# Kernel tuning notes

Measured on AMD Instinct MI355X. Metric: run time of the kernel, lower is better.

Reference implementation:

```python
import jax, jax.numpy as jnp
import numpy as np

NEG_NUM = -10000.0

def setup_inputs() -> dict:
    key = jax.random.key(0)
    k1, k2, k3, k4, k5, k6 = jax.random.split(key, 6)
    batch, enc_len = 32, 2048
    ctx_size, query_size, att_hid = 1024, 1024, 512
    in_dim = ctx_size + query_size
    ctx = jax.random.normal(k1, (batch, enc_len, ctx_size), dtype=jnp.float32)
    query = jax.random.normal(k2, (batch, query_size), dtype=jnp.float32)
    mask = jax.random.randint(k3, (batch, enc_len), 0, 2, dtype=jnp.int32)
    # Linear params (stored as (in, out) for x @ W + b)
    s1 = 1.0 / np.sqrt(in_dim)
    W1 = jax.random.uniform(k4, (in_dim, att_hid), jnp.float32, -s1, s1)
    b1 = jnp.zeros((att_hid,), jnp.float32)
    s2 = 1.0 / np.sqrt(att_hid)
    W2 = jax.random.uniform(k5, (att_hid, 1), jnp.float32, -s2, s2)
    b2 = jnp.zeros((1,), jnp.float32)
    return {"ctx": ctx, "query": query, "W1": W1, "b1": b1, "W2": W2, "b2": b2, "mask": mask}

def reference(ctx, query, W1, b1, W2, b2, mask):
    # ctx: (B, S, Dc), query: (B, Dq)
    B, S, Dc = ctx.shape
    Dq = query.shape[-1]
    # Equivalent to concat([ctx, query_expanded]) @ W1: split W1 into ctx/query blocks
    Wc, Wq = W1[:Dc], W1[Dc:]
    hidden = jnp.tanh(jnp.einsum('bsd,dh->bsh', ctx, Wc)
                      + (query @ Wq)[:, None, :] + b1)      # (B, S, H)
    score = jnp.einsum('bsh,h->bs', hidden, W2[:, 0]) + b2[0]  # (B, S)
    score = jnp.where(mask == 0, NEG_NUM, score)
    p_ctx = jax.nn.softmax(score, axis=-1)                   # (B, S)
    expected_ctx = jnp.einsum('bs,bsd->bd', p_ctx, ctx)      # (B, Dc)
    return (expected_ctx, p_ctx)
```

## Files before the change

kernel.cpp:

```cpp
#include <hip/hip_runtime.h>

typedef __bf16 bf16;
typedef __attribute__((ext_vector_type(8))) __bf16 bf16x8;
typedef __attribute__((ext_vector_type(4))) __bf16 bf16x4;
typedef __attribute__((ext_vector_type(4))) float f32x4;

#define B_  32
#define S_  2048
#define DC  1024
#define DQ  1024
#define H_  512
#define M_  (B_*S_)

#define BM  128
#define BN  512
#define BK  32
#define NCH 32

#define GLD16(g, l) __builtin_amdgcn_global_load_lds( \
    (__attribute__((address_space(1))) void*)(g),     \
    (__attribute__((address_space(3))) void*)(l), 16, 0, 0)

__global__ __launch_bounds__(256) void k_prep(const float* __restrict__ W1,
                                              const float* __restrict__ query,
                                              const float* __restrict__ b1,
                                              bf16* __restrict__ WcT2,
                                              float* __restrict__ qb) {
    const int bid = blockIdx.x, tid = threadIdx.x;
    if (bid < 256) {
        __shared__ bf16 t[32 * 68];
        const int kb = bid >> 3;
        const int cb = bid & 7;
        #pragma unroll
        for (int i = 0; i < 2; ++i) {
            int idx = i * 256 + tid;
            int k  = idx >> 4;
            int h4 = (idx & 15) * 4;
            const float4 v = *(const float4*)(W1 + ((size_t)(kb * 32 + k)) * H_ + cb * 64 + h4);
            bf16x4 pk = { (bf16)v.x, (bf16)v.y, (bf16)v.z, (bf16)v.w };
            *(bf16x4*)(&t[k * 68 + h4]) = pk;
        }
        __syncthreads();
        const int col = tid >> 2;
        const int kk0 = (tid & 3) * 8;
        bf16x8 o;
        #pragma unroll
        for (int j = 0; j < 8; ++j) o[j] = t[(kk0 + j) * 68 + col];
        const int kk0s = kk0 ^ (((col >> 1) & 3) << 3);
        *(bf16x8*)(WcT2 + (size_t)kb * 16384 + (size_t)(cb * 64 + col) * 32 + kk0s) = o;
    } else {
        const int r = bid - 256;
        const int hblk = r & 7;
        const int b    = r >> 3;
        __shared__ float q[DQ];
        __shared__ float red[256];
        #pragma unroll
        for (int i = 0; i < 4; ++i)
            q[tid + i * 256] = query[(size_t)b * DQ + tid + i * 256];
        __syncthreads();
        const int h  = hblk * 64 + (tid & 63);
        const int kc = tid >> 6;
        const float* w = W1 + (size_t)DC * H_ + (size_t)(kc * 256) * H_ + h;
        const float* qv = q + kc * 256;
        float acc = 0.0f;
        #pragma unroll 8
        for (int k = 0; k < 256; ++k)
            acc = fmaf(qv[k], w[(size_t)k * H_], acc);
        red[tid] = acc;
        __syncthreads();
        if (tid < 64)
            qb[(size_t)b * H_ + hblk * 64 + tid] =
                red[tid] + red[tid + 64] + red[tid + 128] + red[tid + 192] + b1[hblk * 64 + tid];
    }
}

__global__ __launch_bounds__(512, 2) void k_gemm(const float* __restrict__ ctx,
                                                 const bf16*  __restrict__ WcT2,
                                                 const float* __restrict__ qb,
                                                 const float* __restrict__ W2,
                                                 float* __restrict__ score) {
    __shared__ char smem_raw[147456];
    float* Af = (float*)smem_raw;
    bf16*  Bh = (bf16*)(smem_raw + 49152);
    float* red = (float*)smem_raw;

    const int tid  = threadIdx.x;
    const int mblk = blockIdx.x;
    const size_t row_base = (size_t)mblk * BM;
    const int b = mblk >> 4;

    const int lane = tid & 63;
    const int wv   = tid >> 6;
    const int wm   = wv & 1;
    const int wn   = wv >> 1;
    const int l16  = lane & 15;
    const int quad = lane >> 4;

    f32x4 acc[4][8] = {};

    const int arow0  = wv * 8 + (lane >> 3);
    const int acolsw = ((lane & 7) ^ ((lane >> 3) & 7)) * 4;
    const float* asrc0 = ctx + (row_base + arow0) * (size_t)DC + acolsw;
    const float* asrc1 = asrc0 + (size_t)64 * DC;
    const int adst0 = wv * 256 + lane * 4;
    const int adst1 = adst0 + 2048;
    const bf16* bsrcB = WcT2 + tid * 8;
    const int  boff   = tid * 8;

    const int a0 = (wm * 64 + l16) * 32 + (((quad * 2) ^ (l16 & 7)) * 4);
    const int b0 = (wn * 128 + l16) * 32 + ((quad * 8) ^ (((l16 >> 1) & 3) << 3));

#define KSTEP(KB, RD, WR, ISSUE)                                               \
  {                                                                            \
    if (ISSUE) {                                                               \
      _Pragma("unroll")                                                        \
      for (int i = 0; i < 4; ++i)                                              \
        GLD16(bsrcB + (size_t)((KB) + 2) * 16384 + i * 4096,                   \
              Bh + (WR) * 16384 + boff + i * 4096);                            \
      GLD16(asrc0 + (size_t)((KB) + 2) * 32, Af + (WR) * 4096 + adst0);        \
      GLD16(asrc1 + (size_t)((KB) + 2) * 32, Af + (WR) * 4096 + adst1);        \
    }                                                                          \
    bf16x8 aF[4], bF[8];                                                       \
    _Pragma("unroll")                                                          \
    for (int mf = 0; mf < 4; ++mf) {                                           \
      const f32x4 lo = *(const f32x4*)(Af + (RD) * 4096 + (a0 + mf * 512));    \
      const f32x4 hi = *(const f32x4*)(Af + (RD) * 4096 + ((a0 ^ 4) + mf * 512)); \
      bf16x8 t;                                                                \
      t[0] = (bf16)lo[0]; t[1] = (bf16)lo[1]; t[2] = (bf16)lo[2]; t[3] = (bf16)lo[3]; \
      t[4] = (bf16)hi[0]; t[5] = (bf16)hi[1]; t[6] = (bf16)hi[2]; t[7] = (bf16)hi[3]; \
      aF[mf] = t;                                                              \
    }                                                                          \
    _Pragma("unroll")                                                          \
    for (int nf = 0; nf < 8; ++nf)                                             \
      bF[nf] = *(const bf16x8*)(Bh + (RD) * 16384 + (b0 + nf * 512));          \
    __builtin_amdgcn_s_setprio(1);                                             \
    _Pragma("unroll")                                                          \
    for (int mf = 0; mf < 4; ++mf)                                             \
      _Pragma("unroll")                                                        \
      for (int nf = 0; nf < 8; ++nf)                                           \
        acc[mf][nf] = __builtin_amdgcn_mfma_f32_16x16x32_bf16(aF[mf], bF[nf],  \
                                                              acc[mf][nf], 0, 0, 0); \
    __builtin_amdgcn_s_setprio(0);                                             \
  }

#define WAITBAR(N)                                                             \
    asm volatile("s_waitcnt vmcnt(" #N ")" ::: "memory");                      \
    __builtin_amdgcn_s_barrier();                                              \
    __builtin_amdgcn_sched_barrier(0);

    #pragma unroll
    for (int i = 0; i < 4; ++i)
        GLD16(bsrcB + i * 4096, Bh + boff + i * 4096);
    GLD16(asrc0, Af + adst0);
    GLD16(asrc1, Af + adst1);
    #pragma unroll
    for (int i = 0; i < 4; ++i)
        GLD16(bsrcB + 16384 + i * 4096, Bh + 16384 + boff + i * 4096);
    GLD16(asrc0 + 32, Af + 4096 + adst0);
    GLD16(asrc1 + 32, Af + 4096 + adst1);
    WAITBAR(6)

    #pragma unroll 1
    for (int t3 = 0; t3 < 10; ++t3) {
        const int kb = t3 * 3;
        KSTEP(kb + 0, 0, 2, 1)
        WAITBAR(6)
        KSTEP(kb + 1, 1, 0, 1)
        WAITBAR(6)
        KSTEP(kb + 2, 2, 1, 1)
        WAITBAR(6)
    }
    KSTEP(30, 0, 0, 0)
    asm volatile("s_waitcnt vmcnt(0)" ::: "memory");
    __builtin_amdgcn_s_barrier();
    __builtin_amdgcn_sched_barrier(0);
    KSTEP(31, 1, 0, 0)
    __syncthreads();

#undef KSTEP
#undef WAITBAR

    float qv[8], wvv[8];
    #pragma unroll
    for (int nf = 0; nf < 8; ++nf) {
        int c = wn * 128 + nf * 16 + l16;
        qv[nf]  = qb[(size_t)b * H_ + c];
        wvv[nf] = W2[c];
    }
    #pragma unroll
    for (int mf = 0; mf < 4; ++mf) {
        #pragma unroll
        for (int r = 0; r < 4; ++r) {
            float s = 0.0f;
            #pragma unroll
            for (int nf = 0; nf < 8; ++nf) {
                float x = acc[mf][nf][r] + qv[nf];
                float t = 1.0f - 2.0f / (1.0f + __expf(2.0f * x));
                s = fmaf(t, wvv[nf], s);
            }
            s += __shfl_xor(s, 1);
            s += __shfl_xor(s, 2);
            s += __shfl_xor(s, 4);
            s += __shfl_xor(s, 8);
            if (l16 == 0)
                red[(wm * 64 + mf * 16 + quad * 4 + r) * 4 + wn] = s;
        }
    }
    __syncthreads();
    if (tid < BM)
        score[row_base + tid] = red[tid * 4] + red[tid * 4 + 1] + red[tid * 4 + 2] + red[tid * 4 + 3];
}

__global__ __launch_bounds__(256) void k_softmax(const float* __restrict__ score,
                                                 const float* __restrict__ b2,
                                                 const int*   __restrict__ mask,
                                                 float* __restrict__ p_out) {
    int b = blockIdx.x, tid = threadIdx.x;
    __shared__ float red[256];
    float loc[8];
    float b2v = b2[0];
    float mx = -1e30f;
    #pragma unroll
    for (int i = 0; i < 8; ++i) {
        size_t r = (size_t)b * S_ + i * 256 + tid;
        float v = score[r] + b2v;
        if (mask[r] == 0) v = -10000.0f;
        loc[i] = v;
        mx = fmaxf(mx, v);
    }
    red[tid] = mx; __syncthreads();
    for (int o = 128; o > 0; o >>= 1) {
        if (tid < o) red[tid] = fmaxf(red[tid], red[tid + o]);
        __syncthreads();
    }
    mx = red[0]; __syncthreads();
    float se = 0.0f;
    #pragma unroll
    for (int i = 0; i < 8; ++i) {
        float e = __expf(loc[i] - mx);
        loc[i] = e;
        se += e;
    }
    red[tid] = se; __syncthreads();
    for (int o = 128; o > 0; o >>= 1) {
        if (tid < o) red[tid] += red[tid + o];
        __syncthreads();
    }
    float inv = 1.0f / red[0];
    #pragma unroll
    for (int i = 0; i < 8; ++i)
        p_out[(size_t)b * S_ + i * 256 + tid] = loc[i] * inv;
}

__global__ __launch_bounds__(256) void k_expected(const float* __restrict__ ctx,
                                                  const float* __restrict__ p,
                                                  float* __restrict__ partial) {
    int b = blockIdx.x, ch = blockIdx.y, tid = threadIdx.x;
    __shared__ float ps[64];
    if (tid < 64) ps[tid] = p[(size_t)b * S_ + ch * 64 + tid];
    __syncthreads();
    const float* base = ctx + ((size_t)b * S_ + ch * 64) * DC + tid * 4;
    float ax = 0.f, ay = 0.f, az = 0.f, aw = 0.f;
    #pragma unroll 8
    for (int s = 0; s < 64; ++s) {
        const float4 v = *(const float4*)(base + (size_t)s * DC);
        float w = ps[s];
        ax = fmaf(w, v.x, ax);
        ay = fmaf(w, v.y, ay);
        az = fmaf(w, v.z, az);
        aw = fmaf(w, v.w, aw);
    }
    float4 o = { ax, ay, az, aw };
    *(float4*)(partial + ((size_t)(b * NCH + ch)) * DC + tid * 4) = o;
}

__global__ __launch_bounds__(256) void k_reduce(const float* __restrict__ partial,
                                                float* __restrict__ out) {
    int b = blockIdx.x, tid = threadIdx.x;
    float4 acc = { 0.f, 0.f, 0.f, 0.f };
    #pragma unroll
    for (int c = 0; c < NCH; ++c) {
        const float4 v = *(const float4*)(partial + ((size_t)(b * NCH + c)) * DC + tid * 4);
        acc.x += v.x; acc.y += v.y; acc.z += v.z; acc.w += v.w;
    }
    *(float4*)(out + (size_t)b * DC + tid * 4) = acc;
}

extern "C" void kernel_launch(void* const* d_in, const int* in_sizes, int n_in,
                              void* d_out, int out_size, void* d_ws, size_t ws_size,
                              hipStream_t stream) {
    (void)in_sizes; (void)n_in; (void)out_size; (void)ws_size;
    const float* ctx   = (const float*)d_in[0];
    const float* query = (const float*)d_in[1];
    const float* W1    = (const float*)d_in[2];
    const float* b1    = (const float*)d_in[3];
    const float* W2    = (const float*)d_in[4];
    const float* b2    = (const float*)d_in[5];
    const int*   mask  = (const int*)d_in[6];

    float* out      = (float*)d_out;
    float* expected = out;
    float* p_out    = out + 32768;

    char* w = (char*)d_ws;
    bf16*  WcT2      = (bf16*)w;
    float* qb        = (float*)(w + (1 << 20));
    float* score     = (float*)(w + (1 << 20) + (64 << 10));
    float* partial_e = (float*)(w + (1 << 20) + (320 << 10));

    k_prep    <<<512, 256, 0, stream>>>(W1, query, b1, WcT2, qb);
    k_gemm    <<<512, 512, 0, stream>>>(ctx, WcT2, qb, W2, score);
    k_softmax <<<B_, 256, 0, stream>>>(score, b2, mask, p_out);
    k_expected<<<dim3(B_, NCH), 256, 0, stream>>>(ctx, p_out, partial_e);
    k_reduce  <<<B_, 256, 0, stream>>>(partial_e, expected);
}
```

Before: 480.1 us.

## Compact unmasked rows and skip masked positions in GEMM and weighted sum

A new prep stage builds a per-batch list of unmasked sequence indices and counts via a prefix scan. The GEMM and expected-context kernels then process only those rows, gathering ctx rows through the index list, because masked scores are overwritten and their softmax weights underflow to zero. The aim is to roughly halve both the ctx traffic and the MFMA work. In exchange, A tiles are loaded straight into registers instead of through LDS, and the B swizzle is dropped, which may cause LDS bank conflicts. If a batch were fully masked, the results would differ from the uniform-softmax reference.

```diff
diff --git a/kernel.cpp b/kernel.cpp
--- a/kernel.cpp
+++ b/kernel.cpp
@@ -10,12 +10,8 @@
 #define DC  1024
 #define DQ  1024
 #define H_  512
-#define M_  (B_*S_)
-
-#define BM  128
-#define BN  512
-#define BK  32
-#define NCH 32
+#define NCH 16
+#define NBLK 16
 
 #define GLD16(g, l) __builtin_amdgcn_global_load_lds( \
     (__attribute__((address_space(1))) void*)(g),     \
@@ -24,8 +20,11 @@
 __global__ __launch_bounds__(256) void k_prep(const float* __restrict__ W1,
                                               const float* __restrict__ query,
                                               const float* __restrict__ b1,
+                                              const int*   __restrict__ mask,
                                               bf16* __restrict__ WcT2,
-                                              float* __restrict__ qb) {
+                                              float* __restrict__ qb,
+                                              int* __restrict__ glist,
+                                              int* __restrict__ cnts) {
     const int bid = blockIdx.x, tid = threadIdx.x;
     if (bid < 256) {
         __shared__ bf16 t[32 * 68];
@@ -46,9 +45,8 @@
         bf16x8 o;
         #pragma unroll
         for (int j = 0; j < 8; ++j) o[j] = t[(kk0 + j) * 68 + col];
-        const int kk0s = kk0 ^ (((col >> 1) & 3) << 3);
-        *(bf16x8*)(WcT2 + (size_t)kb * 16384 + (size_t)(cb * 64 + col) * 32 + kk0s) = o;
-    } else {
+        *(bf16x8*)(WcT2 + (size_t)kb * 16384 + (size_t)(cb * 64 + col) * 32 + kk0) = o;
+    } else if (bid < 512) {
         const int r = bid - 256;
         const int hblk = r & 7;
         const int b    = r >> 3;
@@ -71,6 +69,32 @@
         if (tid < 64)
             qb[(size_t)b * H_ + hblk * 64 + tid] =
                 red[tid] + red[tid + 64] + red[tid + 128] + red[tid + 192] + b1[hblk * 64 + tid];
+    } else {
+        const int b = bid - 512;
+        __shared__ int sc[256];
+        int c = 0;
+        #pragma unroll
+        for (int i = 0; i < 8; ++i)
+            if (mask[(size_t)b * S_ + tid * 8 + i] != 0) ++c;
+        sc[tid] = c;
+        __syncthreads();
+        for (int o = 1; o < 256; o <<= 1) {
+            int v = sc[tid];
+            int u = (tid >= o) ? sc[tid - o] : 0;
+            __syncthreads();
+            sc[tid] = v + u;
+            __syncthreads();
+        }
+        const int total = sc[255];
+        int w = sc[tid] - c;
+        for (int i = 0; i < 8; ++i) {
+            int s = tid * 8 + i;
+            if (mask[(size_t)b * S_ + s] != 0)
+                glist[(size_t)b * S_ + (w++)] = b * S_ + s;
+        }
+        for (int pos = total + tid; pos < S_; pos += 256)
+            glist[(size_t)b * S_ + pos] = b * S_;
+        if (tid == 0) cnts[b] = total;
     }
 }
 
@@ -78,16 +102,18 @@
                                                  const bf16*  __restrict__ WcT2,
                                                  const float* __restrict__ qb,
                                                  const float* __restrict__ W2,
+                                                 const int*   __restrict__ glist,
+                                                 const int*   __restrict__ cnts,
                                                  float* __restrict__ score) {
-    __shared__ char smem_raw[147456];
-    float* Af = (float*)smem_raw;
-    bf16*  Bh = (bf16*)(smem_raw + 49152);
-    float* red = (float*)smem_raw;
-
-    const int tid  = threadIdx.x;
-    const int mblk = blockIdx.x;
-    const size_t row_base = (size_t)mblk * BM;
-    const int b = mblk >> 4;
+    __shared__ char smem[98304 + 2048];
+    bf16*  Bh  = (bf16*)smem;
+    float* red = (float*)(smem + 98304);
+
+    const int tid = threadIdx.x;
+    const int b   = blockIdx.x >> 4;
+    const int blk = blockIdx.x & (NBLK - 1);
+    const int cnt = cnts[b];
+    if (blk * 128 >= cnt) return;
 
     const int lane = tid & 63;
     const int wv   = tid >> 6;
@@ -96,43 +122,61 @@
     const int l16  = lane & 15;
     const int quad = lane >> 4;
 
+    const int* lrow = glist + (size_t)b * S_ + blk * 128 + wm * 64 + l16;
+    const float* ap[4];
+    #pragma unroll
+    for (int mf = 0; mf < 4; ++mf)
+        ap[mf] = ctx + (size_t)lrow[mf * 16] * DC + quad * 8;
+
+    const bf16* bsrc = WcT2 + tid * 8;
+    const int   boff = tid * 8;
+    const int   b0   = (wn * 128 + l16) * 32 + quad * 8;
+
     f32x4 acc[4][8] = {};
-
-    const int arow0  = wv * 8 + (lane >> 3);
-    const int acolsw = ((lane & 7) ^ ((lane >> 3) & 7)) * 4;
-    const float* asrc0 = ctx + (row_base + arow0) * (size_t)DC + acolsw;
-    const float* asrc1 = asrc0 + (size_t)64 * DC;
-    const int adst0 = wv * 256 + lane * 4;
-    const int adst1 = adst0 + 2048;
-    const bf16* bsrcB = WcT2 + tid * 8;
-    const int  boff   = tid * 8;
-
-    const int a0 = (wm * 64 + l16) * 32 + (((quad * 2) ^ (l16 & 7)) * 4);
-    const int b0 = (wn * 128 + l16) * 32 + ((quad * 8) ^ (((l16 >> 1) & 3) << 3));
-
-#define KSTEP(KB, RD, WR, ISSUE)                                               \
+    float4 alo[4], ahi[4];
+
+    #pragma unroll
+    for (int mf = 0; mf < 4; ++mf) {
+        alo[mf] = *(const float4*)(ap[mf]);
+        ahi[mf] = *(const float4*)(ap[mf] + 4);
+    }
+    #pragma unroll
+    for (int i = 0; i < 4; ++i) GLD16(bsrc + i * 4096, Bh + boff + i * 4096);
+    #pragma unroll
+    for (int i = 0; i < 4; ++i) GLD16(bsrc + 16384 + i * 4096, Bh + 16384 + boff + i * 4096);
+    asm volatile("s_waitcnt vmcnt(4)" ::: "memory");
+    __builtin_amdgcn_s_barrier();
+    __builtin_amdgcn_sched_barrier(0);
+
+#define KSTEP(KB, RD, WR)                                                      \
   {                                                                            \
-    if (ISSUE) {                                                               \
+    bf16x8 aF[4];                                                              \
+    _Pragma("unroll")                                                          \
+    for (int mf = 0; mf < 4; ++mf) {                                           \
+      bf16x8 t;                                                                \
+      t[0]=(bf16)alo[mf].x; t[1]=(bf16)alo[mf].y;                              \
+      t[2]=(bf16)alo[mf].z; t[3]=(bf16)alo[mf].w;                              \
+      t[4]=(bf16)ahi[mf].x; t[5]=(bf16)ahi[mf].y;                              \
+      t[6]=(bf16)ahi[mf].z; t[7]=(bf16)ahi[mf].w;                              \
+      aF[mf] = t;                                                              \
+    }                                                                          \
+    if ((KB) < 31) {                                                           \
+      _Pragma("unroll")                                                        \
+      for (int mf = 0; mf < 4; ++mf) {                                         \
+        alo[mf] = *(const float4*)(ap[mf] + ((KB) + 1) * 32);                  \
+        ahi[mf] = *(const float4*)(ap[mf] + ((KB) + 1) * 32 + 4);              \
+      }                                                                        \
+    }                                                                          \
+    if ((KB) < 30) {                                                           \
       _Pragma("unroll")                                                        \
       for (int i = 0; i < 4; ++i)                                              \
-        GLD16(bsrcB + (size_t)((KB) + 2) * 16384 + i * 4096,                   \
+        GLD16(bsrc + (size_t)((KB) + 2) * 16384 + i * 4096,                    \
               Bh + (WR) * 16384 + boff + i * 4096);                            \
-      GLD16(asrc0 + (size_t)((KB) + 2) * 32, Af + (WR) * 4096 + adst0);        \
-      GLD16(asrc1 + (size_t)((KB) + 2) * 32, Af + (WR) * 4096 + adst1);        \
     }                                                                          \
-    bf16x8 aF[4], bF[8];                                                       \
-    _Pragma("unroll")                                                          \
-    for (int mf = 0; mf < 4; ++mf) {                                           \
-      const f32x4 lo = *(const f32x4*)(Af + (RD) * 4096 + (a0 + mf * 512));    \
-      const f32x4 hi = *(const f32x4*)(Af + (RD) * 4096 + ((a0 ^ 4) + mf * 512)); \
-      bf16x8 t;                                                                \
-      t[0] = (bf16)lo[0]; t[1] = (bf16)lo[1]; t[2] = (bf16)lo[2]; t[3] = (bf16)lo[3]; \
-      t[4] = (bf16)hi[0]; t[5] = (bf16)hi[1]; t[6] = (bf16)hi[2]; t[7] = (bf16)hi[3]; \
-      aF[mf] = t;                                                              \
-    }                                                                          \
+    bf16x8 bF[8];                                                              \
     _Pragma("unroll")                                                          \
     for (int nf = 0; nf < 8; ++nf)                                             \
-      bF[nf] = *(const bf16x8*)(Bh + (RD) * 16384 + (b0 + nf * 512));          \
+      bF[nf] = *(const bf16x8*)(Bh + (RD) * 16384 + b0 + nf * 512);            \
     __builtin_amdgcn_s_setprio(1);                                             \
     _Pragma("unroll")                                                          \
     for (int mf = 0; mf < 4; ++mf)                                             \
@@ -148,34 +192,15 @@
     __builtin_amdgcn_s_barrier();                                              \
     __builtin_amdgcn_sched_barrier(0);
 
-    #pragma unroll
-    for (int i = 0; i < 4; ++i)
-        GLD16(bsrcB + i * 4096, Bh + boff + i * 4096);
-    GLD16(asrc0, Af + adst0);
-    GLD16(asrc1, Af + adst1);
-    #pragma unroll
-    for (int i = 0; i < 4; ++i)
-        GLD16(bsrcB + 16384 + i * 4096, Bh + 16384 + boff + i * 4096);
-    GLD16(asrc0 + 32, Af + 4096 + adst0);
-    GLD16(asrc1 + 32, Af + 4096 + adst1);
-    WAITBAR(6)
-
     #pragma unroll 1
     for (int t3 = 0; t3 < 10; ++t3) {
-        const int kb = t3 * 3;
-        KSTEP(kb + 0, 0, 2, 1)
-        WAITBAR(6)
-        KSTEP(kb + 1, 1, 0, 1)
-        WAITBAR(6)
-        KSTEP(kb + 2, 2, 1, 1)
-        WAITBAR(6)
-    }
-    KSTEP(30, 0, 0, 0)
-    asm volatile("s_waitcnt vmcnt(0)" ::: "memory");
-    __builtin_amdgcn_s_barrier();
-    __builtin_amdgcn_sched_barrier(0);
-    KSTEP(31, 1, 0, 0)
-    __syncthreads();
+        KSTEP(t3 * 3 + 0, 0, 2) WAITBAR(12)
+        KSTEP(t3 * 3 + 1, 1, 0) WAITBAR(12)
+        KSTEP(t3 * 3 + 2, 2, 1) WAITBAR(12)
+    }
+    KSTEP(30, 0, 0)
+    WAITBAR(8)
+    KSTEP(31, 1, 0)
 
 #undef KSTEP
 #undef WAITBAR
@@ -207,8 +232,13 @@
         }
     }
     __syncthreads();
-    if (tid < BM)
-        score[row_base + tid] = red[tid * 4] + red[tid * 4 + 1] + red[tid * 4 + 2] + red[tid * 4 + 3];
+    if (tid < 128) {
+        int pos = blk * 128 + tid;
+        if (pos < cnt) {
+            float s = red[tid * 4] + red[tid * 4 + 1] + red[tid * 4 + 2] + red[tid * 4 + 3];
+            score[glist[(size_t)b * S_ + pos]] = s;
+        }
+    }
 }
 
 __global__ __launch_bounds__(256) void k_softmax(const float* __restrict__ score,
@@ -254,16 +284,26 @@
 
 __global__ __launch_bounds__(256) void k_expected(const float* __restrict__ ctx,
                                                   const float* __restrict__ p,
+                                                  const int*   __restrict__ glist,
+                                                  const int*   __restrict__ cnts,
                                                   float* __restrict__ partial) {
     int b = blockIdx.x, ch = blockIdx.y, tid = threadIdx.x;
-    __shared__ float ps[64];
-    if (tid < 64) ps[tid] = p[(size_t)b * S_ + ch * 64 + tid];
+    const int cnt = cnts[b];
+    const int n0 = ch * 128;
+    int nloc = cnt - n0;
+    if (nloc > 128) nloc = 128;
+    __shared__ float ps[128];
+    __shared__ int   gi[128];
+    if (tid < 128) {
+        int g = glist[(size_t)b * S_ + n0 + tid];
+        gi[tid] = g;
+        ps[tid] = (n0 + tid < cnt) ? p[g] : 0.0f;
+    }
     __syncthreads();
-    const float* base = ctx + ((size_t)b * S_ + ch * 64) * DC + tid * 4;
     float ax = 0.f, ay = 0.f, az = 0.f, aw = 0.f;
-    #pragma unroll 8
-    for (int s = 0; s < 64; ++s) {
-        const float4 v = *(const float4*)(base + (size_t)s * DC);
+    #pragma unroll 4
+    for (int s = 0; s < nloc; ++s) {
+        const float4 v = *(const float4*)(ctx + (size_t)gi[s] * DC + tid * 4);
         float w = ps[s];
         ax = fmaf(w, v.x, ax);
         ay = fmaf(w, v.y, ay);
@@ -306,11 +346,13 @@
     bf16*  WcT2      = (bf16*)w;
     float* qb        = (float*)(w + (1 << 20));
     float* score     = (float*)(w + (1 << 20) + (64 << 10));
-    float* partial_e = (float*)(w + (1 << 20) + (320 << 10));
-
-    k_prep    <<<512, 256, 0, stream>>>(W1, query, b1, WcT2, qb);
-    k_gemm    <<<512, 512, 0, stream>>>(ctx, WcT2, qb, W2, score);
+    int*   glist     = (int*)  (w + (1 << 20) + (320 << 10));
+    int*   cnts      = (int*)  (w + (1 << 20) + (576 << 10));
+    float* partial_e = (float*)(w + (2 << 20));
+
+    k_prep    <<<544, 256, 0, stream>>>(W1, query, b1, mask, WcT2, qb, glist, cnts);
+    k_gemm    <<<B_ * NBLK, 512, 0, stream>>>(ctx, WcT2, qb, W2, glist, cnts, score);
     k_softmax <<<B_, 256, 0, stream>>>(score, b2, mask, p_out);
-    k_expected<<<dim3(B_, NCH), 256, 0, stream>>>(ctx, p_out, partial_e);
+    k_expected<<<dim3(B_, NCH), 256, 0, stream>>>(ctx, p_out, glist, cnts, partial_e);
     k_reduce  <<<B_, 256, 0, stream>>>(partial_e, expected);
 }
```

New measurement: 571.9 us. +19.1%, slower.
